# Performance work log

Hardware: AMD Instinct MI355X
Metric: run time of the kernel (lower is better)

The kernel has to match this reference:

```python
import jax, jax.numpy as jnp
import numpy as np

# Module hyperparameters (init_kwargs)
K_VAL = 1.0        # Lorentz curvature parameter k (manifold origin time = 1/sqrt(k))
KSIZE = 9
STRIDE = 1
PAD = 4
B, C, L = 32, 16, 16384   # batch, in_channels (incl. time coord), length
OUT_CH = 64
CONCAT_DIM = 1 + (C - 1) * KSIZE  # 136


def setup_inputs() -> dict:
    key = jax.random.key(0)
    k1, k2 = jax.random.split(key, 2)
    # Build valid Lorentz points: channel 0 is the time coordinate,
    # x0 = sqrt(1/k + ||x_space||^2) so that each length position lies on the manifold.
    space = jax.random.normal(k1, (B, C - 1, L), dtype=jnp.float32)
    time = jnp.sqrt(1.0 / K_VAL + jnp.sum(space * space, axis=1, keepdims=True))
    x = jnp.concatenate([time, space], axis=1)  # [B, C, L]
    # Lorentz FC params: weight maps concat_dim -> (out_channels - 1) spatial dims;
    # the output time coordinate is recomputed from the space norm.
    W = jax.random.normal(k2, (OUT_CH - 1, CONCAT_DIM), dtype=jnp.float32) * (1.0 / np.sqrt(CONCAT_DIM))
    b = jnp.zeros((OUT_CH - 1,), dtype=jnp.float32)
    return {"x": x, "W": W, "b": b}


def reference(x, W, b):
    batch, c, length = x.shape
    k, s, p = KSIZE, STRIDE, PAD
    inv_sqrt_k = (1.0 / K_VAL) ** 0.5
    # Pad with the Lorentz origin: time coord = 1/sqrt(k), space coords = 0
    pad_time = jnp.full((batch, 1, p), inv_sqrt_k, dtype=x.dtype)
    pad_space = jnp.zeros((batch, c - 1, p), dtype=x.dtype)
    pad_block = jnp.concatenate([pad_time, pad_space], axis=1)  # [B, C, p]
    xp = jnp.concatenate([pad_block, x, pad_block], axis=2)     # [B, C, L+2p]
    l_pad = length + 2 * p
    num_patches = (l_pad - k) // s + 1
    # im2col unfold: overlapping windows of size k along length
    idx = jnp.arange(num_patches)[:, None] * s + jnp.arange(k)[None, :]  # [P, k]
    patches = xp[:, :, idx]                      # [B, C, P, k]
    patches = jnp.transpose(patches, (0, 2, 3, 1))  # [B, P, k, C]
    # Lorentz direct_concat: concat spatial parts of the k points, recompute time
    space = patches[..., 1:].reshape(batch, num_patches, k * (c - 1))  # [B, P, (C-1)*k]
    time = jnp.sqrt(1.0 / K_VAL + jnp.sum(space * space, axis=-1, keepdims=True))
    concat = jnp.concatenate([time, space], axis=-1)  # [B, P, concat_dim]
    # Lorentz FC ('ours'): space = relu(W x + b); time = sqrt(1/k + ||space||^2)
    h = jax.nn.relu(jnp.einsum('bpd,od->bpo', concat, W) + b)  # [B, P, OUT_CH-1]
    t_out = jnp.sqrt(1.0 / K_VAL + jnp.sum(h * h, axis=-1, keepdims=True))
    out = jnp.concatenate([t_out, h], axis=-1)  # [B, P, OUT_CH]
    return jnp.transpose(out, (0, 2, 1))        # [B, OUT_CH, P]
```

## Files before the change

kernel.cpp:

```cpp
#include <hip/hip_runtime.h>
#include <math.h>

typedef __bf16 bf16x8 __attribute__((ext_vector_type(8)));
typedef float f32x4 __attribute__((ext_vector_type(4)));
typedef unsigned short u16t;

namespace {
constexpr int B_ = 32, CIN = 16, CSP = 15, L_ = 16384;
constexpr int KS = 9, PAD = 4, OUTC = 64, NW = 63, CD = 136;
constexpr int PP = 256;
constexpr int KT = 160;
constexpr int NKS = 5;
constexpr int XR = 268;
constexpr int RSTR = 24;
constexpr int HTP = 68;

constexpr int OFF_XT = 0;
constexpr int OFF_CSQ = OFF_XT + XR * RSTR * 2;
constexpr int OFF_HT = ((OFF_CSQ + XR * 4 + 15) / 16) * 16;
constexpr int OFF_RED = OFF_HT + 4 * 16 * HTP * 4;
constexpr int LDS_BYTES = OFF_RED + 4 * PP * 4;
static_assert(LDS_BYTES <= 64 * 1024, "LDS overflow");

__device__ inline u16t f2bf(float v) {
  unsigned ui = __float_as_uint(v);
  return (u16t)((ui + 0x7fffu + ((ui >> 16) & 1u)) >> 16);
}
__device__ inline float bf2f(u16t u) { return __uint_as_float(((unsigned)u) << 16); }
}

__global__ void prep_w(const float* __restrict__ W, u16t* __restrict__ wbf) {
  int i = blockIdx.x * 256 + threadIdx.x;
  if (i >= OUTC * KT) return;
  int o = i / KT, kk = i - o * KT;
  int jt = kk >> 4, cs = kk & 15;
  float v = 0.f;
  if (o < NW && jt < KS && cs < CSP) v = W[o * CD + 1 + jt * CSP + cs];
  wbf[i] = f2bf(v);
}

__global__ __launch_bounds__(256, 4)
void lorentz_mfma(const float* __restrict__ x, const float* __restrict__ W,
                  const float* __restrict__ bias, const u16t* __restrict__ wbf,
                  float* __restrict__ out) {
  __shared__ __align__(16) char lds[LDS_BYTES];
  const int tid = threadIdx.x;
  const int b = blockIdx.y;
  const int p0 = blockIdx.x * PP;
  const int wv = tid >> 6;
  const int lane = tid & 63;
  const int q = lane >> 4, r = lane & 15;
  const int jtq = q >> 1, half = q & 1;
  const int row = 16 * wv + r;

  u16t* Xt = (u16t*)(lds + OFF_XT);
  float* csq = (float*)(lds + OFF_CSQ);
  float* ht = (float*)(lds + OFF_HT) + wv * 16 * HTP;
  float* red = (float*)(lds + OFF_RED);

  uint4 wfrag[NKS];
#pragma unroll
  for (int ks = 0; ks < NKS; ++ks)
    wfrag[ks] = *(const uint4*)(wbf + row * KT + ks * 32 + q * 8);
  const float w0v = (row < NW) ? W[row * CD] : 0.f;
  const float bv = (row < NW) ? bias[row] : 0.f;

  for (int t = tid; t < XR; t += 256) Xt[t * RSTR + 15] = 0;
  for (int e4 = tid; e4 < CSP * (XR / 4); e4 += 256) {
    int cs = e4 / (XR / 4);
    int t4 = e4 - cs * (XR / 4);
    int t = 4 * t4;
    int g0 = p0 - PAD + t;
    const float* src = x + ((size_t)b * CIN + cs + 1) * L_ + g0;
    float v0, v1, v2, v3;
    if (g0 >= 0 && g0 + 3 < L_) {
      float4 v = *(const float4*)src;
      v0 = v.x; v1 = v.y; v2 = v.z; v3 = v.w;
    } else {
      v0 = (g0 >= 0 && g0 < L_) ? src[0] : 0.f;
      v1 = (g0 + 1 >= 0 && g0 + 1 < L_) ? src[1] : 0.f;
      v2 = (g0 + 2 >= 0 && g0 + 2 < L_) ? src[2] : 0.f;
      v3 = (g0 + 3 >= 0 && g0 + 3 < L_) ? src[3] : 0.f;
    }
    u16t* dst = Xt + t * RSTR + cs;
    dst[0] = f2bf(v0);
    dst[RSTR] = f2bf(v1);
    dst[2 * RSTR] = f2bf(v2);
    dst[3 * RSTR] = f2bf(v3);
  }
  __syncthreads();

  for (int t = tid; t < XR; t += 256) {
    const uint4* rw4 = (const uint4*)(Xt + t * RSTR);
    uint4 a = rw4[0], c = rw4[1];
    unsigned wds[8] = {a.x, a.y, a.z, a.w, c.x, c.y, c.z, c.w};
    float s = 0.f;
#pragma unroll
    for (int i = 0; i < 8; ++i) {
      float lo = bf2f((u16t)(wds[i] & 0xffffu));
      float hi = bf2f((u16t)(wds[i] >> 16));
      s = fmaf(lo, lo, s);
      s = fmaf(hi, hi, s);
    }
    csq[t] = s;
  }
  __syncthreads();

  const int cl = lane >> 4;
  const int pj = lane & 15;
  for (int grp = 0; grp < 4; ++grp) {
    f32x4 hreg[4];
#pragma unroll
    for (int sl = 0; sl < 4; ++sl) {
      const int s = grp * 4 + sl;
      bf16x8 av[NKS];
#pragma unroll
      for (int ks = 0; ks < NKS; ++ks) {
        int xrow = s * 16 + r + 2 * ks + jtq;
        av[ks] = *(const bf16x8*)(lds + OFF_XT + xrow * (RSTR * 2) + half * 16);
      }
      f32x4 accA = {0.f, 0.f, 0.f, 0.f}, accB = {0.f, 0.f, 0.f, 0.f};
      {
        union { uint4 u; bf16x8 v; } w0, w1, w2, w3, w4;
        w0.u = wfrag[0]; w1.u = wfrag[1]; w2.u = wfrag[2];
        w3.u = wfrag[3]; w4.u = wfrag[4];
        accA = __builtin_amdgcn_mfma_f32_16x16x32_bf16(av[0], w0.v, accA, 0, 0, 0);
        accB = __builtin_amdgcn_mfma_f32_16x16x32_bf16(av[1], w1.v, accB, 0, 0, 0);
        accA = __builtin_amdgcn_mfma_f32_16x16x32_bf16(av[2], w2.v, accA, 0, 0, 0);
        accB = __builtin_amdgcn_mfma_f32_16x16x32_bf16(av[3], w3.v, accB, 0, 0, 0);
        accA = __builtin_amdgcn_mfma_f32_16x16x32_bf16(av[4], w4.v, accA, 0, 0, 0);
      }
      const f32x4 acc = accA + accB;

      const int base = s * 16 + q * 4;
      const f32x4* c4 = (const f32x4*)(csq + base);
      f32x4 ca = c4[0], cm = c4[1], cc = c4[2];
      float v[12] = {ca[0], ca[1], ca[2], ca[3], cm[0], cm[1], cm[2], cm[3],
                     cc[0], cc[1], cc[2], cc[3]};
      float ws0 = ((v[0] + v[1]) + (v[2] + v[3])) + ((v[4] + v[5]) + (v[6] + v[7])) + v[8];
      float ws1 = ws0 - v[0] + v[9];
      float ws2 = ws1 - v[1] + v[10];
      float ws3 = ws2 - v[2] + v[11];
      const float wsv[4] = {ws0, ws1, ws2, ws3};
      f32x4 hh;
#pragma unroll
      for (int g = 0; g < 4; ++g) {
        float tmg = sqrtf(1.f + wsv[g]);
        hh[g] = fmaxf(fmaf(w0v, tmg, acc[g]) + bv, 0.f);
      }
      hreg[sl] = hh;
    }

#pragma unroll
    for (int sl = 0; sl < 4; ++sl)
      *(f32x4*)(ht + r * HTP + sl * 16 + q * 4) = hreg[sl];

    f32x4 ps = {0.f, 0.f, 0.f, 0.f};
#pragma unroll
    for (int j = 0; j < 4; ++j) {
      const int rw = 4 * j + cl;
      f32x4 hv = *(const f32x4*)(ht + rw * HTP + pj * 4);
      ps += hv * hv;
      const int oc = 16 * wv + rw;
      if (oc < NW) {
        *(float4*)(out + ((size_t)b * OUTC + oc + 1) * L_ + p0 + grp * 64 + pj * 4) =
            make_float4(hv[0], hv[1], hv[2], hv[3]);
      }
    }
#pragma unroll
    for (int g = 0; g < 4; ++g) {
      ps[g] += __shfl_xor(ps[g], 16, 64);
      ps[g] += __shfl_xor(ps[g], 32, 64);
    }
    if (lane < 16)
      *(f32x4*)(red + wv * PP + grp * 64 + lane * 4) = ps;
  }
  __syncthreads();

  if (wv == 0) {
    const f32x4* r4 = (const f32x4*)red;
    f32x4 s0 = r4[lane], s1 = r4[64 + lane], s2 = r4[128 + lane], s3 = r4[192 + lane];
    float4 t;
    t.x = sqrtf(1.f + s0[0] + s1[0] + s2[0] + s3[0]);
    t.y = sqrtf(1.f + s0[1] + s1[1] + s2[1] + s3[1]);
    t.z = sqrtf(1.f + s0[2] + s1[2] + s2[2] + s3[2]);
    t.w = sqrtf(1.f + s0[3] + s1[3] + s2[3] + s3[3]);
    *(float4*)(out + (size_t)b * OUTC * L_ + p0 + 4 * lane) = t;
  }
}

extern "C" void kernel_launch(void* const* d_in, const int* in_sizes, int n_in,
                              void* d_out, int out_size, void* d_ws, size_t ws_size,
                              hipStream_t stream) {
  const float* x = (const float*)d_in[0];
  const float* W = (const float*)d_in[1];
  const float* bias = (const float*)d_in[2];
  float* out = (float*)d_out;
  u16t* wbf = (u16t*)d_ws;

  hipLaunchKernelGGL(prep_w, dim3((OUTC * KT + 255) / 256), dim3(256), 0, stream, W, wbf);
  hipLaunchKernelGGL(lorentz_mfma, dim3(L_ / PP, B_), dim3(256), 0, stream,
                     x, W, bias, wbf, out);
}
```

Measured before the change: 48.43 us.

## Fuse weight bf16 conversion into main kernel and shrink reduction LDS

Removes the separate prep_w launch. Each wave now converts its own weight fragments from fp32 to bf16 directly from W, which saves one kernel launch and the workspace round-trip. The per-wave time-coordinate partial sums now go through LDS atomicAdd into a single PP-sized buffer instead of four per-wave buffers. That shrinks LDS so launch bounds can be raised to 5 blocks per CU. The trade-off is redundant scalar weight loads and conversions in every block, plus the cost of LDS atomics.

```diff
diff --git a/kernel.cpp b/kernel.cpp
--- a/kernel.cpp
+++ b/kernel.cpp
@@ -9,7 +9,6 @@
 constexpr int B_ = 32, CIN = 16, CSP = 15, L_ = 16384;
 constexpr int KS = 9, PAD = 4, OUTC = 64, NW = 63, CD = 136;
 constexpr int PP = 256;
-constexpr int KT = 160;
 constexpr int NKS = 5;
 constexpr int XR = 268;
 constexpr int RSTR = 24;
@@ -19,8 +18,8 @@
 constexpr int OFF_CSQ = OFF_XT + XR * RSTR * 2;
 constexpr int OFF_HT = ((OFF_CSQ + XR * 4 + 15) / 16) * 16;
 constexpr int OFF_RED = OFF_HT + 4 * 16 * HTP * 4;
-constexpr int LDS_BYTES = OFF_RED + 4 * PP * 4;
-static_assert(LDS_BYTES <= 64 * 1024, "LDS overflow");
+constexpr int LDS_BYTES = OFF_RED + PP * 4;
+static_assert(LDS_BYTES <= 32 * 1024 + 512, "LDS overflow");
 
 __device__ inline u16t f2bf(float v) {
   unsigned ui = __float_as_uint(v);
@@ -29,20 +28,9 @@
 __device__ inline float bf2f(u16t u) { return __uint_as_float(((unsigned)u) << 16); }
 }
 
-__global__ void prep_w(const float* __restrict__ W, u16t* __restrict__ wbf) {
-  int i = blockIdx.x * 256 + threadIdx.x;
-  if (i >= OUTC * KT) return;
-  int o = i / KT, kk = i - o * KT;
-  int jt = kk >> 4, cs = kk & 15;
-  float v = 0.f;
-  if (o < NW && jt < KS && cs < CSP) v = W[o * CD + 1 + jt * CSP + cs];
-  wbf[i] = f2bf(v);
-}
-
-__global__ __launch_bounds__(256, 4)
+__global__ __launch_bounds__(256, 5)
 void lorentz_mfma(const float* __restrict__ x, const float* __restrict__ W,
-                  const float* __restrict__ bias, const u16t* __restrict__ wbf,
-                  float* __restrict__ out) {
+                  const float* __restrict__ bias, float* __restrict__ out) {
   __shared__ __align__(16) char lds[LDS_BYTES];
   const int tid = threadIdx.x;
   const int b = blockIdx.y;
@@ -59,28 +47,46 @@
   float* red = (float*)(lds + OFF_RED);
 
   uint4 wfrag[NKS];
-#pragma unroll
-  for (int ks = 0; ks < NKS; ++ks)
-    wfrag[ks] = *(const uint4*)(wbf + row * KT + ks * 32 + q * 8);
+  {
+    const float* wr = W + (size_t)row * CD;
+#pragma unroll
+    for (int ks = 0; ks < NKS; ++ks) {
+      const int jt = 2 * ks + jtq;
+      union { u16t h[8]; uint4 u; } pk;
+      if (row < NW && jt < KS) {
+        const float* src = wr + 1 + jt * CSP + 8 * half;
+#pragma unroll
+        for (int e = 0; e < 8; ++e) {
+          float v = (8 * half + e < CSP) ? src[e] : 0.f;
+          pk.h[e] = f2bf(v);
+        }
+      } else {
+        pk.u = make_uint4(0, 0, 0, 0);
+      }
+      wfrag[ks] = pk.u;
+    }
+  }
   const float w0v = (row < NW) ? W[row * CD] : 0.f;
   const float bv = (row < NW) ? bias[row] : 0.f;
 
-  for (int t = tid; t < XR; t += 256) Xt[t * RSTR + 15] = 0;
-  for (int e4 = tid; e4 < CSP * (XR / 4); e4 += 256) {
+  red[tid] = 0.f;
+  for (int e4 = tid; e4 < 16 * (XR / 4); e4 += 256) {
     int cs = e4 / (XR / 4);
     int t4 = e4 - cs * (XR / 4);
     int t = 4 * t4;
     int g0 = p0 - PAD + t;
-    const float* src = x + ((size_t)b * CIN + cs + 1) * L_ + g0;
-    float v0, v1, v2, v3;
-    if (g0 >= 0 && g0 + 3 < L_) {
-      float4 v = *(const float4*)src;
-      v0 = v.x; v1 = v.y; v2 = v.z; v3 = v.w;
-    } else {
-      v0 = (g0 >= 0 && g0 < L_) ? src[0] : 0.f;
-      v1 = (g0 + 1 >= 0 && g0 + 1 < L_) ? src[1] : 0.f;
-      v2 = (g0 + 2 >= 0 && g0 + 2 < L_) ? src[2] : 0.f;
-      v3 = (g0 + 3 >= 0 && g0 + 3 < L_) ? src[3] : 0.f;
+    float v0 = 0.f, v1 = 0.f, v2 = 0.f, v3 = 0.f;
+    if (cs < CSP) {
+      const float* src = x + ((size_t)b * CIN + cs + 1) * L_ + g0;
+      if (g0 >= 0 && g0 + 3 < L_) {
+        float4 v = *(const float4*)src;
+        v0 = v.x; v1 = v.y; v2 = v.z; v3 = v.w;
+      } else {
+        v0 = (g0 >= 0 && g0 < L_) ? src[0] : 0.f;
+        v1 = (g0 + 1 >= 0 && g0 + 1 < L_) ? src[1] : 0.f;
+        v2 = (g0 + 2 >= 0 && g0 + 2 < L_) ? src[2] : 0.f;
+        v3 = (g0 + 3 >= 0 && g0 + 3 < L_) ? src[3] : 0.f;
+      }
     }
     u16t* dst = Xt + t * RSTR + cs;
     dst[0] = f2bf(v0);
@@ -172,19 +178,18 @@
       ps[g] += __shfl_xor(ps[g], 16, 64);
       ps[g] += __shfl_xor(ps[g], 32, 64);
     }
-    if (lane < 16)
-      *(f32x4*)(red + wv * PP + grp * 64 + lane * 4) = ps;
+    float pval = (cl == 0) ? ps[0] : (cl == 1) ? ps[1] : (cl == 2) ? ps[2] : ps[3];
+    atomicAdd(&red[grp * 64 + pj * 4 + cl], pval);
   }
   __syncthreads();
 
   if (wv == 0) {
-    const f32x4* r4 = (const f32x4*)red;
-    f32x4 s0 = r4[lane], s1 = r4[64 + lane], s2 = r4[128 + lane], s3 = r4[192 + lane];
+    const f32x4 s4 = *(const f32x4*)(red + 4 * lane);
     float4 t;
-    t.x = sqrtf(1.f + s0[0] + s1[0] + s2[0] + s3[0]);
-    t.y = sqrtf(1.f + s0[1] + s1[1] + s2[1] + s3[1]);
-    t.z = sqrtf(1.f + s0[2] + s1[2] + s2[2] + s3[2]);
-    t.w = sqrtf(1.f + s0[3] + s1[3] + s2[3] + s3[3]);
+    t.x = sqrtf(1.f + s4[0]);
+    t.y = sqrtf(1.f + s4[1]);
+    t.z = sqrtf(1.f + s4[2]);
+    t.w = sqrtf(1.f + s4[3]);
     *(float4*)(out + (size_t)b * OUTC * L_ + p0 + 4 * lane) = t;
   }
 }
@@ -196,9 +201,6 @@
   const float* W = (const float*)d_in[1];
   const float* bias = (const float*)d_in[2];
   float* out = (float*)d_out;
-  u16t* wbf = (u16t*)d_ws;
-
-  hipLaunchKernelGGL(prep_w, dim3((OUTC * KT + 255) / 256), dim3(256), 0, stream, W, wbf);
   hipLaunchKernelGGL(lorentz_mfma, dim3(L_ / PP, B_), dim3(256), 0, stream,
-                     x, W, bias, wbf, out);
-}
+                     x, W, bias, out);
+}
```

After: 54.03 us. +11.6%, slower.
